# Kernel tuning notes

Measured on AMD Instinct MI355X. Metric: run time of the kernel, lower is better.

## Reference

```python
import jax, jax.numpy as jnp
import numpy as np

N_STEPS = 8  # fixed-step RK4 over t in [0, 1]


def setup_inputs() -> dict:
    key = jax.random.key(0)
    ks = jax.random.split(key, 5)
    B, T, F, C = 64, 4096, 76, 15
    x = jax.random.normal(ks[0], (B, T, F), dtype=jnp.float32)
    # Conv1d(76->76, k=3) weights, PyTorch OIH layout, fan-in scaled
    conv_w = jax.random.normal(ks[1], (F, F, 3), dtype=jnp.float32) * (1.0 / np.sqrt(F * 3))
    conv_b = jax.random.normal(ks[2], (F,), dtype=jnp.float32) * 0.01
    final_w = jax.random.normal(ks[3], (C, F), dtype=jnp.float32) * (1.0 / np.sqrt(F))
    final_b = jax.random.normal(ks[4], (C,), dtype=jnp.float32) * 0.01
    return {"x": x, "conv_w": conv_w, "conv_b": conv_b,
            "final_w": final_w, "final_b": final_b}


def _func(h, conv_w, conv_b):
    # h: [B, F, T]; Conv1d k=3 pad=1 -> Tanh (the ODE vector field)
    y = jax.lax.conv_general_dilated(
        h, conv_w, window_strides=(1,), padding=[(1, 1)],
        dimension_numbers=("NCH", "OIH", "NCH"))
    return jnp.tanh(y + conv_b[None, :, None])


def reference(x, conv_w, conv_b, final_w, final_b):
    # x: [B, T, F] -> permute to channels-first for Conv1d
    h0 = jnp.transpose(x, (0, 2, 1))  # [B, F, T]
    dt = jnp.float32(1.0 / N_STEPS)

    def rk4_step(h, _):
        k1 = _func(h, conv_w, conv_b)
        k2 = _func(h + 0.5 * dt * k1, conv_w, conv_b)
        k3 = _func(h + 0.5 * dt * k2, conv_w, conv_b)
        k4 = _func(h + dt * k3, conv_w, conv_b)
        return h + (dt / 6.0) * (k1 + 2.0 * k2 + 2.0 * k3 + k4), None

    hT, _ = jax.lax.scan(rk4_step, h0, None, length=N_STEPS)
    # back to [B, T, F], then final Linear(F -> num_classes)
    out = jnp.einsum("bft,cf->btc", hT, final_w) + final_b
    return out
```

## Files before the change

kernel.cpp:

```cpp
#include <hip/hip_runtime.h>
#include <cstdint>
#include <cstddef>

#define F_CH 76
#define T_LEN 4096
#define B_TOT 64
#define C_CLS 15
#define NSTEP 8

#define W_OUT  120
#define HALO   4
#define NBT    35
#define NKB    5
#define SSTR   88
#define SROWS  130
#define TPB    768
#define HP     80

#define C2LOG2E 2.8853900817779268f

typedef __attribute__((ext_vector_type(8)))  __bf16 bf16x8;
typedef __attribute__((ext_vector_type(4)))  __bf16 bf16x4;
typedef __attribute__((ext_vector_type(16))) float  f32x16;

__global__ __launch_bounds__(256) void pad_copy_kernel(
    const float* __restrict__ x, float* __restrict__ h, int b0)
{
    int bl = blockIdx.y;
    int q  = blockIdx.x * 256 + threadIdx.x;
    int t  = q / 20, c4 = (q - t * 20) * 4;
    float4 v = {0.f, 0.f, 0.f, 0.f};
    if (c4 < F_CH)
        v = *(const float4*)(x + ((size_t)(b0 + bl) * T_LEN + t) * F_CH + c4);
    *(float4*)(h + ((size_t)bl * T_LEN + t) * HP + c4) = v;
}

__global__ __launch_bounds__(256) void wprep_kernel(
    const float* __restrict__ cw, __bf16* __restrict__ wpb)
{
    int idx = blockIdx.x * 256 + threadIdx.x;
    if (idx >= 3 * 96 * SSTR) return;
    int tap = idx / (96 * SSTR);
    int rem = idx - tap * 96 * SSTR;
    int c = rem / SSTR, ci = rem - c * SSTR;
    float v = 0.0f;
    if (c < F_CH && ci < F_CH) v = cw[((size_t)c * F_CH + ci) * 3 + tap];
    wpb[idx] = (__bf16)v;
}

__global__ __launch_bounds__(TPB, 3) void rk4_step_kernel(
    const float* __restrict__ hin, float* __restrict__ hout,
    const __bf16* __restrict__ wpb, const float* __restrict__ cb)
{
    __shared__ __bf16 s_lds[2][SROWS][SSTR];
    __shared__ float  cb_lds[96];

    const int b    = blockIdx.y;
    const int T0   = blockIdx.x * W_OUT;
    const int tid  = threadIdx.x;
    const int lane = tid & 63;
    const int l31  = lane & 31;
    const int l5   = lane >> 5;
    const int wv   = tid >> 6;
    const int ct   = wv >> 2;
    const int tq   = wv & 3;
    const bool ct2 = (__builtin_amdgcn_readfirstlane(ct) == 2);

    const int  rb  = tq * 32 + l31;
    const int  t   = T0 - HALO + rb;
    const bool tok = (t >= 0 && t < T_LEN);

    if (tid < 176) {
        int bi = tid / 88, rr = (tid % 88) / 44, c = tid % 44;
        ((uint32_t*)&s_lds[bi][rr ? (SROWS - 1) : 0][0])[c] = 0u;
    }
    if (tid < 96) cb_lds[tid] = (tid < F_CH) ? cb[tid] * C2LOG2E : 0.0f;

    float h_reg[16], hn[16];
    const float* hb = hin + (size_t)b * T_LEN * HP;
    #pragma unroll
    for (int q = 0; q < 4; ++q) {
        int c0 = ct * 32 + l5 * 4 + q * 8;
        float4 v = {0.f, 0.f, 0.f, 0.f};
        if (tok && c0 < HP) v = *(const float4*)(hb + (size_t)t * HP + c0);
        h_reg[q * 4 + 0] = v.x; h_reg[q * 4 + 1] = v.y;
        h_reg[q * 4 + 2] = v.z; h_reg[q * 4 + 3] = v.w;
        hn[q * 4 + 0] = v.x; hn[q * 4 + 1] = v.y;
        hn[q * 4 + 2] = v.z; hn[q * 4 + 3] = v.w;
    }

    bf16x8 afr[3][NKB];
    #pragma unroll
    for (int tap = 0; tap < 3; ++tap)
        #pragma unroll
        for (int kb = 0; kb < NKB; ++kb)
            afr[tap][kb] = *(const bf16x8*)&wpb[((size_t)tap * 96 + ct * 32 + l31) * SSTR
                                                + kb * 16 + l5 * 8];

    #pragma unroll
    for (int q = 0; q < 4; ++q) {
        if (ct2 && q >= 2) continue;
        int c0 = ct * 32 + l5 * 4 + q * 8;
        bf16x4 p;
        #pragma unroll
        for (int j = 0; j < 4; ++j) p[j] = (__bf16)h_reg[q * 4 + j];
        *(bf16x4*)&s_lds[0][rb + 1][c0] = p;
    }
    __syncthreads();

    const float dt = 0.125f;
    bf16x4 spack[4];

    #pragma unroll 1
    for (int e = 0; e < 4; ++e) {
        const float we   = (e == 0 || e == 3) ? dt / 6.0f : dt / 3.0f;
        const float al   = (e == 2) ? dt : 0.5f * dt;
        const float al_t = tok ? al : 0.0f;

        const __bf16 (*sb)[SSTR] = s_lds[e & 1];
        f32x16 acc = {};
        #pragma unroll
        for (int tap = 0; tap < 3; ++tap) {
            #pragma unroll
            for (int kb = 0; kb < NKB; ++kb) {
                bf16x8 bf = *(const bf16x8*)&sb[rb + tap][kb * 16 + l5 * 8];
                acc = __builtin_amdgcn_mfma_f32_32x32x16_bf16(afr[tap][kb], bf, acc, 0, 0, 0);
            }
        }

        #pragma unroll
        for (int q = 0; q < 4; ++q) {
            if (ct2 && q >= 2) continue;
            int c0 = ct * 32 + l5 * 4 + q * 8;
            #pragma unroll
            for (int j = 0; j < 4; ++j) {
                float y  = fmaf(acc[q * 4 + j], C2LOG2E, cb_lds[c0 + j]);
                float ex = __builtin_amdgcn_exp2f(y);
                float r  = __builtin_amdgcn_rcpf(ex + 1.0f);
                float kv = fmaf(-2.0f, r, 1.0f);
                hn[q * 4 + j] = fmaf(we, kv, hn[q * 4 + j]);
                if (e < 3) spack[q][j] = (__bf16)fmaf(al_t, kv, h_reg[q * 4 + j]);
            }
        }

        if (e < 3) {
            __bf16 (*sw)[SSTR] = s_lds[(e + 1) & 1];
            #pragma unroll
            for (int q = 0; q < 4; ++q) {
                if (ct2 && q >= 2) continue;
                int c0 = ct * 32 + l5 * 4 + q * 8;
                *(bf16x4*)&sw[rb + 1][c0] = spack[q];
            }
            __syncthreads();
        }
    }

    if (rb >= HALO && rb < HALO + W_OUT && t < T_LEN) {
        float* ho = hout + ((size_t)b * T_LEN + t) * HP;
        #pragma unroll
        for (int q = 0; q < 4; ++q) {
            int c0 = ct * 32 + l5 * 4 + q * 8;
            if (c0 < HP) {
                float4 v;
                v.x = hn[q * 4 + 0]; v.y = hn[q * 4 + 1];
                v.z = hn[q * 4 + 2]; v.w = hn[q * 4 + 3];
                *(float4*)(ho + c0) = v;
            }
        }
    }
}

__global__ __launch_bounds__(256) void final_kernel(
    const float* __restrict__ h, const float* __restrict__ fw,
    const float* __restrict__ fb, float* __restrict__ out, int b0)
{
    int bl = blockIdx.y;
    int t  = blockIdx.x * 256 + threadIdx.x;
    const float* hr = h + ((size_t)bl * T_LEN + t) * HP;
    float acc[C_CLS];
#pragma unroll
    for (int c = 0; c < C_CLS; ++c) acc[c] = fb[c];
#pragma unroll
    for (int qf = 0; qf < 19; ++qf) {
        float4 v = *(const float4*)(hr + qf * 4);
#pragma unroll
        for (int c = 0; c < C_CLS; ++c) {
            const float* w = fw + c * F_CH + qf * 4;
            acc[c] = fmaf(w[0], v.x, acc[c]);
            acc[c] = fmaf(w[1], v.y, acc[c]);
            acc[c] = fmaf(w[2], v.z, acc[c]);
            acc[c] = fmaf(w[3], v.w, acc[c]);
        }
    }
    float* ob = out + ((size_t)(b0 + bl) * T_LEN + t) * C_CLS;
#pragma unroll
    for (int c = 0; c < C_CLS; ++c) ob[c] = acc[c];
}

extern "C" void kernel_launch(void* const* d_in, const int* in_sizes, int n_in,
                              void* d_out, int out_size, void* d_ws, size_t ws_size,
                              hipStream_t stream)
{
    const float* x  = (const float*)d_in[0];
    const float* cw = (const float*)d_in[1];
    const float* cb = (const float*)d_in[2];
    const float* fw = (const float*)d_in[3];
    const float* fb = (const float*)d_in[4];
    float* out = (float*)d_out;

    const size_t FT = (size_t)T_LEN * HP;

    __bf16* WPB = (__bf16*)d_ws;
    const size_t wpbFloats = 12800;
    float* planes = (float*)d_ws + wpbFloats;

    size_t planeBytes = 2 * FT * sizeof(float);
    size_t avail = ws_size - wpbFloats * sizeof(float);
    int Bc = (int)(avail / planeBytes);
    if (Bc > B_TOT) Bc = B_TOT;
    if (Bc < 1) Bc = 1;

    float* H0 = planes;
    float* H1 = H0 + (size_t)Bc * FT;

    wprep_kernel<<<(3 * 96 * SSTR + 255) / 256, 256, 0, stream>>>(cw, WPB);

    for (int b0 = 0; b0 < B_TOT; b0 += Bc) {
        int bc = (B_TOT - b0 < Bc) ? (B_TOT - b0) : Bc;

        dim3 gP(T_LEN * 20 / 256, bc);
        pad_copy_kernel<<<gP, 256, 0, stream>>>(x, H0, b0);

        float* hcur = H0;
        float* hnxt = H1;
        dim3 gR(NBT, bc);
        for (int st = 0; st < NSTEP; ++st) {
            rk4_step_kernel<<<gR, TPB, 0, stream>>>(hcur, hnxt, WPB, cb);
            float* tmp = hcur; hcur = hnxt; hnxt = tmp;
        }

        dim3 gF(T_LEN / 256, bc);
        final_kernel<<<gF, 256, 0, stream>>>(hcur, fw, fb, out, b0);
    }
}
```

Measured before the change: 909.4 us.

## Fuse two RK4 steps per launch with wider halo and two row tiles per wave

The step kernel now runs two full RK4 steps per launch, so the halo doubles (8 rows) and the output window shrinks to 112 rows with 37 time blocks. This halves the number of launches and the global round trips of the state between steps. Each wave now handles two 32-row tiles with 384 threads, so the weight fragments held in registers are reused across twice as many MFMAs. The cost is extra recomputation in the halo, more registers per thread, and a bf16-rounded copy of the stage base state instead of an fp32 one.

```diff
diff --git a/kernel.cpp b/kernel.cpp
--- a/kernel.cpp
+++ b/kernel.cpp
@@ -8,13 +8,13 @@
 #define C_CLS 15
 #define NSTEP 8
 
-#define W_OUT  120
-#define HALO   4
-#define NBT    35
+#define W_OUT  112
+#define HALO2  8
+#define NBT    37
 #define NKB    5
 #define SSTR   88
 #define SROWS  130
-#define TPB    768
+#define TPB    384
 #define HP     80
 
 #define C2LOG2E 2.8853900817779268f
@@ -48,7 +48,7 @@
     wpb[idx] = (__bf16)v;
 }
 
-__global__ __launch_bounds__(TPB, 3) void rk4_step_kernel(
+__global__ __launch_bounds__(TPB, 3) void rk4_step2_kernel(
     const float* __restrict__ hin, float* __restrict__ hout,
     const __bf16* __restrict__ wpb, const float* __restrict__ cb)
 {
@@ -62,13 +62,15 @@
     const int l31  = lane & 31;
     const int l5   = lane >> 5;
     const int wv   = tid >> 6;
-    const int ct   = wv >> 2;
-    const int tq   = wv & 3;
-    const bool ct2 = (__builtin_amdgcn_readfirstlane(ct) == 2);
-
-    const int  rb  = tq * 32 + l31;
-    const int  t   = T0 - HALO + rb;
-    const bool tok = (t >= 0 && t < T_LEN);
+    const int ct   = wv >> 1;
+    const int tth  = wv & 1;
+
+    const int  rb0  = (tth * 2 + 0) * 32 + l31;
+    const int  rb1  = rb0 + 32;
+    const int  t0g  = T0 - HALO2 + rb0;
+    const int  t1g  = T0 - HALO2 + rb1;
+    const bool tok0 = (t0g >= 0 && t0g < T_LEN);
+    const bool tok1 = (t1g >= 0 && t1g < T_LEN);
 
     if (tid < 176) {
         int bi = tid / 88, rr = (tid % 88) / 44, c = tid % 44;
@@ -76,17 +78,23 @@
     }
     if (tid < 96) cb_lds[tid] = (tid < F_CH) ? cb[tid] * C2LOG2E : 0.0f;
 
-    float h_reg[16], hn[16];
+    float  hn0[16], hn1[16];
+    bf16x4 hpk0[4], hpk1[4];
     const float* hb = hin + (size_t)b * T_LEN * HP;
     #pragma unroll
     for (int q = 0; q < 4; ++q) {
         int c0 = ct * 32 + l5 * 4 + q * 8;
-        float4 v = {0.f, 0.f, 0.f, 0.f};
-        if (tok && c0 < HP) v = *(const float4*)(hb + (size_t)t * HP + c0);
-        h_reg[q * 4 + 0] = v.x; h_reg[q * 4 + 1] = v.y;
-        h_reg[q * 4 + 2] = v.z; h_reg[q * 4 + 3] = v.w;
-        hn[q * 4 + 0] = v.x; hn[q * 4 + 1] = v.y;
-        hn[q * 4 + 2] = v.z; hn[q * 4 + 3] = v.w;
+        float4 v0 = {0.f,0.f,0.f,0.f}, v1 = {0.f,0.f,0.f,0.f};
+        if (c0 < HP) {
+            if (tok0) v0 = *(const float4*)(hb + (size_t)t0g * HP + c0);
+            if (tok1) v1 = *(const float4*)(hb + (size_t)t1g * HP + c0);
+        }
+        hn0[q*4+0]=v0.x; hn0[q*4+1]=v0.y; hn0[q*4+2]=v0.z; hn0[q*4+3]=v0.w;
+        hn1[q*4+0]=v1.x; hn1[q*4+1]=v1.y; hn1[q*4+2]=v1.z; hn1[q*4+3]=v1.w;
+        hpk0[q][0]=(__bf16)v0.x; hpk0[q][1]=(__bf16)v0.y;
+        hpk0[q][2]=(__bf16)v0.z; hpk0[q][3]=(__bf16)v0.w;
+        hpk1[q][0]=(__bf16)v1.x; hpk1[q][1]=(__bf16)v1.y;
+        hpk1[q][2]=(__bf16)v1.z; hpk1[q][3]=(__bf16)v1.w;
     }
 
     bf16x8 afr[3][NKB];
@@ -97,74 +105,103 @@
             afr[tap][kb] = *(const bf16x8*)&wpb[((size_t)tap * 96 + ct * 32 + l31) * SSTR
                                                 + kb * 16 + l5 * 8];
 
-    #pragma unroll
-    for (int q = 0; q < 4; ++q) {
-        if (ct2 && q >= 2) continue;
-        int c0 = ct * 32 + l5 * 4 + q * 8;
-        bf16x4 p;
-        #pragma unroll
-        for (int j = 0; j < 4; ++j) p[j] = (__bf16)h_reg[q * 4 + j];
-        *(bf16x4*)&s_lds[0][rb + 1][c0] = p;
-    }
-    __syncthreads();
-
     const float dt = 0.125f;
-    bf16x4 spack[4];
 
     #pragma unroll 1
-    for (int e = 0; e < 4; ++e) {
-        const float we   = (e == 0 || e == 3) ? dt / 6.0f : dt / 3.0f;
-        const float al   = (e == 2) ? dt : 0.5f * dt;
-        const float al_t = tok ? al : 0.0f;
-
-        const __bf16 (*sb)[SSTR] = s_lds[e & 1];
-        f32x16 acc = {};
-        #pragma unroll
-        for (int tap = 0; tap < 3; ++tap) {
-            #pragma unroll
-            for (int kb = 0; kb < NKB; ++kb) {
-                bf16x8 bf = *(const bf16x8*)&sb[rb + tap][kb * 16 + l5 * 8];
-                acc = __builtin_amdgcn_mfma_f32_32x32x16_bf16(afr[tap][kb], bf, acc, 0, 0, 0);
-            }
-        }
-
-        #pragma unroll
-        for (int q = 0; q < 4; ++q) {
-            if (ct2 && q >= 2) continue;
-            int c0 = ct * 32 + l5 * 4 + q * 8;
-            #pragma unroll
-            for (int j = 0; j < 4; ++j) {
-                float y  = fmaf(acc[q * 4 + j], C2LOG2E, cb_lds[c0 + j]);
-                float ex = __builtin_amdgcn_exp2f(y);
-                float r  = __builtin_amdgcn_rcpf(ex + 1.0f);
-                float kv = fmaf(-2.0f, r, 1.0f);
-                hn[q * 4 + j] = fmaf(we, kv, hn[q * 4 + j]);
-                if (e < 3) spack[q][j] = (__bf16)fmaf(al_t, kv, h_reg[q * 4 + j]);
-            }
-        }
-
-        if (e < 3) {
-            __bf16 (*sw)[SSTR] = s_lds[(e + 1) & 1];
-            #pragma unroll
-            for (int q = 0; q < 4; ++q) {
-                if (ct2 && q >= 2) continue;
-                int c0 = ct * 32 + l5 * 4 + q * 8;
-                *(bf16x4*)&sw[rb + 1][c0] = spack[q];
-            }
-            __syncthreads();
-        }
-    }
-
-    if (rb >= HALO && rb < HALO + W_OUT && t < T_LEN) {
-        float* ho = hout + ((size_t)b * T_LEN + t) * HP;
+    for (int st = 0; st < 2; ++st) {
         #pragma unroll
         for (int q = 0; q < 4; ++q) {
             int c0 = ct * 32 + l5 * 4 + q * 8;
             if (c0 < HP) {
-                float4 v;
-                v.x = hn[q * 4 + 0]; v.y = hn[q * 4 + 1];
-                v.z = hn[q * 4 + 2]; v.w = hn[q * 4 + 3];
-                *(float4*)(ho + c0) = v;
+                *(bf16x4*)&s_lds[0][rb0 + 1][c0] = hpk0[q];
+                *(bf16x4*)&s_lds[0][rb1 + 1][c0] = hpk1[q];
+            }
+        }
+        __syncthreads();
+
+        #pragma unroll 1
+        for (int e = 0; e < 4; ++e) {
+            const float we    = (e == 0 || e == 3) ? dt / 6.0f : dt / 3.0f;
+            const float al    = (e == 2) ? dt : 0.5f * dt;
+            const float al_t0 = tok0 ? al : 0.0f;
+            const float al_t1 = tok1 ? al : 0.0f;
+
+            const __bf16 (*sb)[SSTR] = s_lds[e & 1];
+            f32x16 a0 = {}, a1 = {};
+            #pragma unroll
+            for (int tap = 0; tap < 3; ++tap) {
+                #pragma unroll
+                for (int kb = 0; kb < NKB; ++kb) {
+                    bf16x8 bf0 = *(const bf16x8*)&sb[rb0 + tap][kb * 16 + l5 * 8];
+                    bf16x8 bf1 = *(const bf16x8*)&sb[rb1 + tap][kb * 16 + l5 * 8];
+                    a0 = __builtin_amdgcn_mfma_f32_32x32x16_bf16(afr[tap][kb], bf0, a0, 0, 0, 0);
+                    a1 = __builtin_amdgcn_mfma_f32_32x32x16_bf16(afr[tap][kb], bf1, a1, 0, 0, 0);
+                }
+            }
+
+            __bf16 (*sw)[SSTR] = s_lds[(e + 1) & 1];
+            #pragma unroll
+            for (int q = 0; q < 4; ++q) {
+                int c0 = ct * 32 + l5 * 4 + q * 8;
+                if (c0 >= HP) continue;
+                bf16x4 p0, p1;
+                #pragma unroll
+                for (int j = 0; j < 4; ++j) {
+                    float bia = cb_lds[c0 + j];
+                    float y0  = fmaf(a0[q*4+j], C2LOG2E, bia);
+                    float y1  = fmaf(a1[q*4+j], C2LOG2E, bia);
+                    float ex0 = __builtin_amdgcn_exp2f(y0);
+                    float ex1 = __builtin_amdgcn_exp2f(y1);
+                    float kv0 = fmaf(-2.0f, __builtin_amdgcn_rcpf(ex0 + 1.0f), 1.0f);
+                    float kv1 = fmaf(-2.0f, __builtin_amdgcn_rcpf(ex1 + 1.0f), 1.0f);
+                    hn0[q*4+j] = fmaf(we, kv0, hn0[q*4+j]);
+                    hn1[q*4+j] = fmaf(we, kv1, hn1[q*4+j]);
+                    if (e < 3) {
+                        p0[j] = (__bf16)fmaf(al_t0, kv0, (float)hpk0[q][j]);
+                        p1[j] = (__bf16)fmaf(al_t1, kv1, (float)hpk1[q][j]);
+                    }
+                }
+                if (e < 3) {
+                    *(bf16x4*)&sw[rb0 + 1][c0] = p0;
+                    *(bf16x4*)&sw[rb1 + 1][c0] = p1;
+                }
+            }
+            if (e < 3) __syncthreads();
+        }
+
+        if (st == 0) {
+            #pragma unroll
+            for (int i = 0; i < 16; ++i) {
+                hn0[i] = tok0 ? hn0[i] : 0.0f;
+                hn1[i] = tok1 ? hn1[i] : 0.0f;
+            }
+            #pragma unroll
+            for (int q = 0; q < 4; ++q) {
+                #pragma unroll
+                for (int j = 0; j < 4; ++j) {
+                    hpk0[q][j] = (__bf16)hn0[q*4+j];
+                    hpk1[q][j] = (__bf16)hn1[q*4+j];
+                }
+            }
+        }
+    }
+
+    float* ho = hout + (size_t)b * T_LEN * HP;
+    #pragma unroll
+    for (int u = 0; u < 2; ++u) {
+        int   rbu = u ? rb1 : rb0;
+        int   tg  = u ? t1g : t0g;
+        const float* hnu = u ? hn1 : hn0;
+        if (rbu >= HALO2 && rbu < HALO2 + W_OUT && tg < T_LEN) {
+            #pragma unroll
+            for (int q = 0; q < 4; ++q) {
+                int c0 = ct * 32 + l5 * 4 + q * 8;
+                if (c0 < HP) {
+                    float4 v;
+                    v.x = hnu[q*4+0]; v.y = hnu[q*4+1];
+                    v.z = hnu[q*4+2]; v.w = hnu[q*4+3];
+                    *(float4*)(ho + (size_t)tg * HP + c0) = v;
+                }
             }
         }
     }
@@ -234,8 +271,8 @@
         float* hcur = H0;
         float* hnxt = H1;
         dim3 gR(NBT, bc);
-        for (int st = 0; st < NSTEP; ++st) {
-            rk4_step_kernel<<<gR, TPB, 0, stream>>>(hcur, hnxt, WPB, cb);
+        for (int st2 = 0; st2 < NSTEP / 2; ++st2) {
+            rk4_step2_kernel<<<gR, TPB, 0, stream>>>(hcur, hnxt, WPB, cb);
             float* tmp = hcur; hcur = hnxt; hnxt = tmp;
         }
 
```

Measured after the change: 877.7 us. -3.5%, faster.

## Fuse two RK4 steps per kernel launch with wider halo and smaller tiles

Applied to the files above, without the earlier changes.

Each kernel launch now advances two RK4 steps, using an 8-row halo and 48 useful output rows per 64-row tile, with 384 threads per block. This halves the global round-trips of the state and the number of launches. In exchange it does redundant halo compute, since 16 of every 64 rows are recomputed, and it keeps the intermediate state only in bf16 between the two fused steps. The work split across waves also changes: 6 waves cover channel tiles by 2 time quarters, and the earlier ct2 special case is dropped in favour of c0<HP checks.

```diff
diff --git a/kernel.cpp b/kernel.cpp
--- a/kernel.cpp
+++ b/kernel.cpp
@@ -8,13 +8,13 @@
 #define C_CLS 15
 #define NSTEP 8
 
-#define W_OUT  120
-#define HALO   4
-#define NBT    35
+#define W_OUT  48
+#define HALO2  8
+#define NBT    86
 #define NKB    5
 #define SSTR   88
-#define SROWS  130
-#define TPB    768
+#define SROWS  66
+#define TPB    384
 #define HP     80
 
 #define C2LOG2E 2.8853900817779268f
@@ -48,7 +48,7 @@
     wpb[idx] = (__bf16)v;
 }
 
-__global__ __launch_bounds__(TPB, 3) void rk4_step_kernel(
+__global__ __launch_bounds__(TPB, 4) void rk4_step2_kernel(
     const float* __restrict__ hin, float* __restrict__ hout,
     const __bf16* __restrict__ wpb, const float* __restrict__ cb)
 {
@@ -62,13 +62,12 @@
     const int l31  = lane & 31;
     const int l5   = lane >> 5;
     const int wv   = tid >> 6;
-    const int ct   = wv >> 2;
-    const int tq   = wv & 3;
-    const bool ct2 = (__builtin_amdgcn_readfirstlane(ct) == 2);
+    const int ct   = wv >> 1;
+    const int tq   = wv & 1;
 
     const int  rb  = tq * 32 + l31;
-    const int  t   = T0 - HALO + rb;
-    const bool tok = (t >= 0 && t < T_LEN);
+    const int  tg  = T0 - HALO2 + rb;
+    const bool tok = (tg >= 0 && tg < T_LEN);
 
     if (tid < 176) {
         int bi = tid / 88, rr = (tid % 88) / 44, c = tid % 44;
@@ -76,17 +75,17 @@
     }
     if (tid < 96) cb_lds[tid] = (tid < F_CH) ? cb[tid] * C2LOG2E : 0.0f;
 
-    float h_reg[16], hn[16];
+    float  hn[16];
+    bf16x4 hpk[4];
     const float* hb = hin + (size_t)b * T_LEN * HP;
     #pragma unroll
     for (int q = 0; q < 4; ++q) {
         int c0 = ct * 32 + l5 * 4 + q * 8;
         float4 v = {0.f, 0.f, 0.f, 0.f};
-        if (tok && c0 < HP) v = *(const float4*)(hb + (size_t)t * HP + c0);
-        h_reg[q * 4 + 0] = v.x; h_reg[q * 4 + 1] = v.y;
-        h_reg[q * 4 + 2] = v.z; h_reg[q * 4 + 3] = v.w;
-        hn[q * 4 + 0] = v.x; hn[q * 4 + 1] = v.y;
-        hn[q * 4 + 2] = v.z; hn[q * 4 + 3] = v.w;
+        if (tok && c0 < HP) v = *(const float4*)(hb + (size_t)tg * HP + c0);
+        hn[q*4+0]=v.x; hn[q*4+1]=v.y; hn[q*4+2]=v.z; hn[q*4+3]=v.w;
+        hpk[q][0]=(__bf16)v.x; hpk[q][1]=(__bf16)v.y;
+        hpk[q][2]=(__bf16)v.z; hpk[q][3]=(__bf16)v.w;
     }
 
     bf16x8 afr[3][NKB];
@@ -97,73 +96,73 @@
             afr[tap][kb] = *(const bf16x8*)&wpb[((size_t)tap * 96 + ct * 32 + l31) * SSTR
                                                 + kb * 16 + l5 * 8];
 
-    #pragma unroll
-    for (int q = 0; q < 4; ++q) {
-        if (ct2 && q >= 2) continue;
-        int c0 = ct * 32 + l5 * 4 + q * 8;
-        bf16x4 p;
-        #pragma unroll
-        for (int j = 0; j < 4; ++j) p[j] = (__bf16)h_reg[q * 4 + j];
-        *(bf16x4*)&s_lds[0][rb + 1][c0] = p;
-    }
-    __syncthreads();
-
     const float dt = 0.125f;
-    bf16x4 spack[4];
 
     #pragma unroll 1
-    for (int e = 0; e < 4; ++e) {
-        const float we   = (e == 0 || e == 3) ? dt / 6.0f : dt / 3.0f;
-        const float al   = (e == 2) ? dt : 0.5f * dt;
-        const float al_t = tok ? al : 0.0f;
-
-        const __bf16 (*sb)[SSTR] = s_lds[e & 1];
-        f32x16 acc = {};
-        #pragma unroll
-        for (int tap = 0; tap < 3; ++tap) {
-            #pragma unroll
-            for (int kb = 0; kb < NKB; ++kb) {
-                bf16x8 bf = *(const bf16x8*)&sb[rb + tap][kb * 16 + l5 * 8];
-                acc = __builtin_amdgcn_mfma_f32_32x32x16_bf16(afr[tap][kb], bf, acc, 0, 0, 0);
-            }
-        }
-
+    for (int st = 0; st < 2; ++st) {
         #pragma unroll
         for (int q = 0; q < 4; ++q) {
-            if (ct2 && q >= 2) continue;
             int c0 = ct * 32 + l5 * 4 + q * 8;
-            #pragma unroll
-            for (int j = 0; j < 4; ++j) {
-                float y  = fmaf(acc[q * 4 + j], C2LOG2E, cb_lds[c0 + j]);
-                float ex = __builtin_amdgcn_exp2f(y);
-                float r  = __builtin_amdgcn_rcpf(ex + 1.0f);
-                float kv = fmaf(-2.0f, r, 1.0f);
-                hn[q * 4 + j] = fmaf(we, kv, hn[q * 4 + j]);
-                if (e < 3) spack[q][j] = (__bf16)fmaf(al_t, kv, h_reg[q * 4 + j]);
+            if (c0 < HP) *(bf16x4*)&s_lds[0][rb + 1][c0] = hpk[q];
+        }
+        __syncthreads();
+
+        #pragma unroll 1
+        for (int e = 0; e < 4; ++e) {
+            const float we   = (e == 0 || e == 3) ? dt / 6.0f : dt / 3.0f;
+            const float al   = (e == 2) ? dt : 0.5f * dt;
+            const float al_t = tok ? al : 0.0f;
+
+            const __bf16 (*sb)[SSTR] = s_lds[e & 1];
+            f32x16 a0 = {};
+            #pragma unroll
+            for (int tap = 0; tap < 3; ++tap) {
+                #pragma unroll
+                for (int kb = 0; kb < NKB; ++kb) {
+                    bf16x8 bf = *(const bf16x8*)&sb[rb + tap][kb * 16 + l5 * 8];
+                    a0 = __builtin_amdgcn_mfma_f32_32x32x16_bf16(afr[tap][kb], bf, a0, 0, 0, 0);
+                }
             }
-        }
-
-        if (e < 3) {
+
             __bf16 (*sw)[SSTR] = s_lds[(e + 1) & 1];
             #pragma unroll
             for (int q = 0; q < 4; ++q) {
-                if (ct2 && q >= 2) continue;
                 int c0 = ct * 32 + l5 * 4 + q * 8;
-                *(bf16x4*)&sw[rb + 1][c0] = spack[q];
+                if (c0 >= HP) continue;
+                bf16x4 p;
+                #pragma unroll
+                for (int j = 0; j < 4; ++j) {
+                    float y  = fmaf(a0[q*4+j], C2LOG2E, cb_lds[c0 + j]);
+                    float ex = __builtin_amdgcn_exp2f(y);
+                    float kv = fmaf(-2.0f, __builtin_amdgcn_rcpf(ex + 1.0f), 1.0f);
+                    hn[q*4+j] = fmaf(we, kv, hn[q*4+j]);
+                    if (e < 3) p[j] = (__bf16)fmaf(al_t, kv, (float)hpk[q][j]);
+                }
+                if (e < 3) *(bf16x4*)&sw[rb + 1][c0] = p;
             }
+            if (e < 3) __syncthreads();
+        }
+
+        if (st == 0) {
+            #pragma unroll
+            for (int i = 0; i < 16; ++i) hn[i] = tok ? hn[i] : 0.0f;
+            #pragma unroll
+            for (int q = 0; q < 4; ++q)
+                #pragma unroll
+                for (int j = 0; j < 4; ++j) hpk[q][j] = (__bf16)hn[q*4+j];
             __syncthreads();
         }
     }
 
-    if (rb >= HALO && rb < HALO + W_OUT && t < T_LEN) {
-        float* ho = hout + ((size_t)b * T_LEN + t) * HP;
+    if (rb >= HALO2 && rb < HALO2 + W_OUT && tg < T_LEN) {
+        float* ho = hout + ((size_t)b * T_LEN + tg) * HP;
         #pragma unroll
         for (int q = 0; q < 4; ++q) {
             int c0 = ct * 32 + l5 * 4 + q * 8;
             if (c0 < HP) {
                 float4 v;
-                v.x = hn[q * 4 + 0]; v.y = hn[q * 4 + 1];
-                v.z = hn[q * 4 + 2]; v.w = hn[q * 4 + 3];
+                v.x = hn[q*4+0]; v.y = hn[q*4+1];
+                v.z = hn[q*4+2]; v.w = hn[q*4+3];
                 *(float4*)(ho + c0) = v;
             }
         }
@@ -234,8 +233,8 @@
         float* hcur = H0;
         float* hnxt = H1;
         dim3 gR(NBT, bc);
-        for (int st = 0; st < NSTEP; ++st) {
-            rk4_step_kernel<<<gR, TPB, 0, stream>>>(hcur, hnxt, WPB, cb);
+        for (int st2 = 0; st2 < NSTEP / 2; ++st2) {
+            rk4_step2_kernel<<<gR, TPB, 0, stream>>>(hcur, hnxt, WPB, cb);
             float* tmp = hcur; hcur = hnxt; hnxt = tmp;
         }
 
```

New measurement: 885.3 us. -2.7%, faster.
